# Optimization experiments

Measured on AMD Instinct MI355X. Metric: run time of the kernel, lower is better.

Reference implementation:

```python
import jax, jax.numpy as jnp
import numpy as np

N_NODES = 100000
N_EDGES = 1600000
F_IN = 32
HIDDEN = 32
N_CLASSES = 2


def setup_inputs() -> dict:
    key = jax.random.key(0)
    k0, k1, k2, k3 = jax.random.split(key, 4)
    x = jax.random.normal(k0, (N_NODES, F_IN), dtype=jnp.float32)
    edge_index = jax.random.randint(k1, (2, N_EDGES), 0, N_NODES, dtype=jnp.int64)
    W1 = jax.random.normal(k2, (F_IN, HIDDEN), dtype=jnp.float32) / np.sqrt(F_IN).astype(np.float32)
    b1 = jnp.zeros((HIDDEN,), dtype=jnp.float32)
    W2 = jax.random.normal(k3, (HIDDEN, N_CLASSES), dtype=jnp.float32) / np.sqrt(HIDDEN).astype(np.float32)
    b2 = jnp.zeros((N_CLASSES,), dtype=jnp.float32)
    return {"x": x, "edge_index": edge_index, "W1": W1, "b1": b1, "W2": W2, "b2": b2}


def _gcn_conv(x, W, b, src, dst, norm, n):
    # linear transform, gather from source nodes, scale by sym-norm, scatter-add to dst
    msg = (x @ W)[src] * norm[:, None]  # [E+N, out]
    return jax.ops.segment_sum(msg, dst, num_segments=n) + b


def reference(x, edge_index, W1, b1, W2, b2):
    n = x.shape[0]
    loops = jnp.arange(n, dtype=edge_index.dtype)
    src = jnp.concatenate([edge_index[0], loops])  # add self-loops (GCNConv default)
    dst = jnp.concatenate([edge_index[1], loops])
    deg = jax.ops.segment_sum(jnp.ones_like(dst, dtype=jnp.float32), dst, num_segments=n)
    dis = jax.lax.rsqrt(jnp.maximum(deg, 1.0))  # deg >= 1 because of self-loops
    norm = dis[src] * dis[dst]  # D^{-1/2} A_hat D^{-1/2} edge weights
    h = jax.nn.relu(_gcn_conv(x, W1, b1, src, dst, norm, n))
    # dropout is identity in eval mode (training=False)
    out = _gcn_conv(h, W2, b2, src, dst, norm, n)
    return jax.nn.log_softmax(out, axis=1)
```

## Files before the change

kernel.cpp:

```cpp
#include <hip/hip_runtime.h>
#include <hip/hip_fp16.h>
#include <math.h>

constexpr int N = 100000;
constexpr int E = 1600000;
constexpr int F = 32;
constexpr int C = 2;

constexpr int NBUCK = (N + 511) >> 9;
constexpr int CAPB  = 10240;
constexpr int CHUNK = 8192;
constexpr int NCHUNK = (E + CHUNK - 1) / CHUNK;

__global__ void k_detect(const int* __restrict__ ei, int* __restrict__ flag,
                         int* __restrict__ bcursor) {
    __shared__ int any;
    if (threadIdx.x == 0) any = 0;
    __syncthreads();
    int acc = 0;
    for (int i = threadIdx.x; i < 2048; i += blockDim.x)
        acc |= ei[2 * i + 1];
    if (acc) atomicOr(&any, 1);
    for (int i = threadIdx.x; i < NBUCK; i += blockDim.x) bcursor[i] = 0;
    __syncthreads();
    if (threadIdx.x == 0) flag[0] = any ? 0 : 1;
}

__device__ __forceinline__ int get_src(const int* ei, int e, int f64) {
    return f64 ? ei[2 * e] : ei[e];
}
__device__ __forceinline__ int get_dst(const int* ei, int e, int f64) {
    return f64 ? ei[2 * (E + e)] : ei[E + e];
}

__global__ void k_bucket(const int* __restrict__ ei, int* __restrict__ bcursor,
                         int* __restrict__ epk, const int* __restrict__ flag) {
    __shared__ int h[NBUCK];
    __shared__ int base[NBUCK];
    __shared__ int sS[CHUNK];
    __shared__ int sD[CHUNK];
    int tid = threadIdx.x;
    for (int i = tid; i < NBUCK; i += blockDim.x) h[i] = 0;
    __syncthreads();
    int f64 = flag[0];
    int e0 = blockIdx.x * CHUNK;
    int ne = min(E - e0, CHUNK);
    for (int i = tid; i < ne; i += blockDim.x) {
        int s = get_src(ei, e0 + i, f64);
        int d = get_dst(ei, e0 + i, f64);
        sS[i] = s;
        sD[i] = d;
        atomicAdd(&h[d >> 9], 1);
    }
    __syncthreads();
    for (int b = tid; b < NBUCK; b += blockDim.x) {
        if (h[b] > 0) base[b] = atomicAdd(&bcursor[b], h[b]);
        h[b] = 0;
    }
    __syncthreads();
    for (int i = tid; i < ne; i += blockDim.x) {
        int d = sD[i];
        int b = d >> 9;
        int r = atomicAdd(&h[b], 1);
        int pos = base[b] + r;
        if (pos < CAPB)
            epk[b * CAPB + pos] = ((d & 511) << 17) | sS[i];
    }
}

__global__ __launch_bounds__(512) void k_csr(
        const int* __restrict__ epk, const int* __restrict__ bcursor,
        int* __restrict__ rs, int* __restrict__ re,
        float* __restrict__ dis, int* __restrict__ colp) {
    __shared__ int hcnt[512];
    __shared__ int s[512];
    __shared__ int lcur[512];
    __shared__ int colseg[CAPB];
    int b = blockIdx.x;
    int tid = threadIdx.x;
    int n0 = b << 9;
    int nn = min(512, N - n0);
    int cbase = b * CAPB;
    int cnt = min(bcursor[b], CAPB);
    hcnt[tid] = 0;
    __syncthreads();
    for (int i = tid; i < cnt; i += 512)
        atomicAdd(&hcnt[epk[cbase + i] >> 17], 1);
    __syncthreads();
    s[tid] = hcnt[tid];
    __syncthreads();
    for (int off = 1; off < 512; off <<= 1) {
        int t = (tid >= off) ? s[tid - off] : 0;
        __syncthreads();
        s[tid] += t;
        __syncthreads();
    }
    int excl = s[tid] - hcnt[tid];
    lcur[tid] = excl;
    if (tid < nn) {
        rs[n0 + tid] = cbase + excl;
        re[n0 + tid] = cbase + excl + hcnt[tid];
        dis[n0 + tid] = rsqrtf((float)(hcnt[tid] + 1));
    }
    __syncthreads();
    for (int i = tid; i < cnt; i += 512) {
        int p = epk[cbase + i];
        int r = atomicAdd(&lcur[p >> 17], 1);
        colseg[r] = p & 0x1FFFF;
    }
    __syncthreads();
    for (int i = tid; i < cnt; i += 512) colp[cbase + i] = colseg[i];
}

__global__ void k_xw1(const float* __restrict__ x, const float* __restrict__ W1,
                      const float* __restrict__ dis, __half* __restrict__ t1h) {
    __shared__ float W1s[F * F];
    int tid = threadIdx.x;
    for (int i = tid; i < F * F; i += blockDim.x) W1s[i] = W1[i];
    __syncthreads();
    int lane = tid & 31;
    int node = (blockIdx.x * blockDim.x + tid) >> 5;
    if (node >= N) return;
    float xv = x[node * F + lane];
    float acc = 0.f;
#pragma unroll
    for (int k = 0; k < F; ++k) acc += __shfl(xv, k, 32) * W1s[k * F + lane];
    float v = acc * dis[node];
    float o = __shfl_xor(v, 1, 32);
    if (!(lane & 1))
        ((__half2*)t1h)[node * 16 + (lane >> 1)] = __floats2half2_rn(v, o);
}

__device__ __forceinline__ void acc8(float4& lo, float4& hi, const float4& r) {
    const __half2* hp = (const __half2*)&r;
    float2 f0 = __half22float2(hp[0]);
    float2 f1 = __half22float2(hp[1]);
    float2 f2 = __half22float2(hp[2]);
    float2 f3 = __half22float2(hp[3]);
    lo.x += f0.x; lo.y += f0.y; lo.z += f1.x; lo.w += f1.y;
    hi.x += f2.x; hi.y += f2.y; hi.z += f3.x; hi.w += f3.y;
}

__global__ void k_agg1(const int* __restrict__ rs, const int* __restrict__ re,
                       const int* __restrict__ colp, const __half* __restrict__ t1h,
                       const float* __restrict__ dis, const float* __restrict__ b1,
                       const float* __restrict__ W2, float* __restrict__ t2) {
    int tid = blockIdx.x * blockDim.x + threadIdx.x;
    int node = tid >> 2;
    if (node >= N) return;
    int lane = tid & 3;
    const float4* t1v = (const float4*)t1h;
    int start = rs[node], end = re[node];
    float4 lo0 = {0,0,0,0}, hi0 = {0,0,0,0};
    float4 lo1 = {0,0,0,0}, hi1 = {0,0,0,0};
    float4 lo2 = {0,0,0,0}, hi2 = {0,0,0,0};
    float4 lo3 = {0,0,0,0}, hi3 = {0,0,0,0};
    for (int base = start; base < end; base += 4) {
        int idx = base + lane;
        int sv = (idx < end) ? colp[idx] : 0;
        int cnt = end - base;
        if (cnt >= 4) {
            int i0 = __shfl(sv, 0, 4);
            int i1 = __shfl(sv, 1, 4);
            int i2 = __shfl(sv, 2, 4);
            int i3 = __shfl(sv, 3, 4);
            float4 r0 = t1v[i0 * 4 + lane];
            float4 r1 = t1v[i1 * 4 + lane];
            float4 r2 = t1v[i2 * 4 + lane];
            float4 r3 = t1v[i3 * 4 + lane];
            acc8(lo0, hi0, r0);
            acc8(lo1, hi1, r1);
            acc8(lo2, hi2, r2);
            acc8(lo3, hi3, r3);
        } else {
            for (int j = 0; j < cnt; ++j) {
                int ss = __shfl(sv, j, 4);
                float4 r = t1v[ss * 4 + lane];
                acc8(lo0, hi0, r);
            }
        }
    }
    float4 alo, ahi;
    alo.x = (lo0.x + lo1.x) + (lo2.x + lo3.x);
    alo.y = (lo0.y + lo1.y) + (lo2.y + lo3.y);
    alo.z = (lo0.z + lo1.z) + (lo2.z + lo3.z);
    alo.w = (lo0.w + lo1.w) + (lo2.w + lo3.w);
    ahi.x = (hi0.x + hi1.x) + (hi2.x + hi3.x);
    ahi.y = (hi0.y + hi1.y) + (hi2.y + hi3.y);
    ahi.z = (hi0.z + hi1.z) + (hi2.z + hi3.z);
    ahi.w = (hi0.w + hi1.w) + (hi2.w + hi3.w);
    float4 wself = t1v[node * 4 + lane];
    const __half2* sp = (const __half2*)&wself;
    float2 s0 = __half22float2(sp[0]);
    float2 s1 = __half22float2(sp[1]);
    float2 s2 = __half22float2(sp[2]);
    float2 s3 = __half22float2(sp[3]);
    float d = dis[node];
    int f0 = 8 * lane;
    float4 b1lo = *(const float4*)(b1 + f0);
    float4 b1hi = *(const float4*)(b1 + f0 + 4);
    float h0 = fmaxf(d * (alo.x + s0.x) + b1lo.x, 0.f);
    float h1 = fmaxf(d * (alo.y + s0.y) + b1lo.y, 0.f);
    float h2 = fmaxf(d * (alo.z + s1.x) + b1lo.z, 0.f);
    float h3 = fmaxf(d * (alo.w + s1.y) + b1lo.w, 0.f);
    float h4 = fmaxf(d * (ahi.x + s2.x) + b1hi.x, 0.f);
    float h5 = fmaxf(d * (ahi.y + s2.y) + b1hi.y, 0.f);
    float h6 = fmaxf(d * (ahi.z + s3.x) + b1hi.z, 0.f);
    float h7 = fmaxf(d * (ahi.w + s3.y) + b1hi.w, 0.f);
    const float4* w2v = (const float4*)W2;
    float4 q0 = w2v[4 * lane + 0];
    float4 q1 = w2v[4 * lane + 1];
    float4 q2 = w2v[4 * lane + 2];
    float4 q3 = w2v[4 * lane + 3];
    float p0 = h0 * q0.x + h1 * q0.z + h2 * q1.x + h3 * q1.z +
               h4 * q2.x + h5 * q2.z + h6 * q3.x + h7 * q3.z;
    float p1 = h0 * q0.y + h1 * q0.w + h2 * q1.y + h3 * q1.w +
               h4 * q2.y + h5 * q2.w + h6 * q3.y + h7 * q3.w;
    p0 += __shfl_xor(p0, 1, 4);
    p0 += __shfl_xor(p0, 2, 4);
    p1 += __shfl_xor(p1, 1, 4);
    p1 += __shfl_xor(p1, 2, 4);
    if (lane == 0) {
        float2 o;
        o.x = p0 * d;
        o.y = p1 * d;
        *(float2*)(t2 + node * C) = o;
    }
}

__global__ void k_agg2(const int* __restrict__ rs, const int* __restrict__ re,
                       const int* __restrict__ colp, const float* __restrict__ t2,
                       const float* __restrict__ dis, const float* __restrict__ b2,
                       float* __restrict__ out) {
    int tid = blockIdx.x * blockDim.x + threadIdx.x;
    int node = tid >> 4;
    if (node >= N) return;
    int lane = tid & 15;
    int start = rs[node], end = re[node];
    float a0 = 0.f, a1 = 0.f;
    for (int idx = start + lane; idx < end; idx += 16) {
        int s = colp[idx];
        float2 v = *(const float2*)(t2 + s * C);
        a0 += v.x;
        a1 += v.y;
    }
#pragma unroll
    for (int off = 8; off > 0; off >>= 1) {
        a0 += __shfl_xor(a0, off, 16);
        a1 += __shfl_xor(a1, off, 16);
    }
    if (lane == 0) {
        float d = dis[node];
        float2 self = *(const float2*)(t2 + node * C);
        float z0 = d * (a0 + self.x) + b2[0];
        float z1 = d * (a1 + self.y) + b2[1];
        float m = fmaxf(z0, z1);
        float l = m + logf(expf(z0 - m) + expf(z1 - m));
        float2 o;
        o.x = z0 - l;
        o.y = z1 - l;
        *(float2*)(out + node * C) = o;
    }
}

extern "C" void kernel_launch(void* const* d_in, const int* in_sizes, int n_in,
                              void* d_out, int out_size, void* d_ws, size_t ws_size,
                              hipStream_t stream) {
    const float* x  = (const float*)d_in[0];
    const int*   ei = (const int*)d_in[1];
    const float* W1 = (const float*)d_in[2];
    const float* b1 = (const float*)d_in[3];
    const float* W2 = (const float*)d_in[4];
    const float* b2 = (const float*)d_in[5];
    float* out = (float*)d_out;

    int* ws_i = (int*)d_ws;
    int*    epk     = ws_i;
    int*    colp    = epk + (size_t)NBUCK * CAPB;
    int*    rs      = colp + (size_t)NBUCK * CAPB;
    int*    re      = rs + N;
    float*  dis     = (float*)(re + N);
    float*  t2      = (float*)(dis + N);
    int*    bcursor = (int*)(t2 + (size_t)N * C);
    int*    flag    = bcursor + NBUCK;
    __half* t1h     = (__half*)epk;

    const int B = 256;
    k_detect<<<1, B, 0, stream>>>(ei, flag, bcursor);
    k_bucket<<<NCHUNK, B, 0, stream>>>(ei, bcursor, epk, flag);
    k_csr<<<NBUCK, 512, 0, stream>>>(epk, bcursor, rs, re, dis, colp);
    k_xw1<<<(N * 32 + B - 1) / B, B, 0, stream>>>(x, W1, dis, t1h);
    k_agg1<<<(N * 4 + B - 1) / B, B, 0, stream>>>(rs, re, colp, t1h, dis, b1, W2, t2);
    k_agg2<<<(N * 16 + B - 1) / B, B, 0, stream>>>(rs, re, colp, t2, dis, b2, out);
}
```

Measured before the change: 109.9 us.

## Fuse dtype detect into bucketing, accumulate agg1 in half2, shrink agg2 groups

Removes the separate detect kernel by having every bucket block check the edge-index dtype itself, and zeroes the bucket cursors with a memset instead. In agg1, neighbour features are summed in packed half2 accumulators and converted to float only at the end, cutting conversion ALU work at the risk of fp16 overflow or precision loss on high-degree nodes. agg2 now uses 8 lanes per node instead of 16. t1h gets its own workspace region rather than aliasing epk.

```diff
diff --git a/kernel.cpp b/kernel.cpp
--- a/kernel.cpp
+++ b/kernel.cpp
@@ -12,20 +12,6 @@
 constexpr int CHUNK = 8192;
 constexpr int NCHUNK = (E + CHUNK - 1) / CHUNK;
 
-__global__ void k_detect(const int* __restrict__ ei, int* __restrict__ flag,
-                         int* __restrict__ bcursor) {
-    __shared__ int any;
-    if (threadIdx.x == 0) any = 0;
-    __syncthreads();
-    int acc = 0;
-    for (int i = threadIdx.x; i < 2048; i += blockDim.x)
-        acc |= ei[2 * i + 1];
-    if (acc) atomicOr(&any, 1);
-    for (int i = threadIdx.x; i < NBUCK; i += blockDim.x) bcursor[i] = 0;
-    __syncthreads();
-    if (threadIdx.x == 0) flag[0] = any ? 0 : 1;
-}
-
 __device__ __forceinline__ int get_src(const int* ei, int e, int f64) {
     return f64 ? ei[2 * e] : ei[e];
 }
@@ -34,15 +20,21 @@
 }
 
 __global__ void k_bucket(const int* __restrict__ ei, int* __restrict__ bcursor,
-                         int* __restrict__ epk, const int* __restrict__ flag) {
+                         int* __restrict__ epk) {
     __shared__ int h[NBUCK];
     __shared__ int base[NBUCK];
     __shared__ int sS[CHUNK];
     __shared__ int sD[CHUNK];
+    __shared__ int sflag;
     int tid = threadIdx.x;
+    if (tid == 0) sflag = 0;
     for (int i = tid; i < NBUCK; i += blockDim.x) h[i] = 0;
     __syncthreads();
-    int f64 = flag[0];
+    int accf = 0;
+    for (int i = tid; i < 2048; i += blockDim.x) accf |= ei[2 * i + 1];
+    if (accf) atomicOr(&sflag, 1);
+    __syncthreads();
+    int f64 = sflag ? 0 : 1;
     int e0 = blockIdx.x * CHUNK;
     int ne = min(E - e0, CHUNK);
     for (int i = tid; i < ne; i += blockDim.x) {
@@ -131,14 +123,12 @@
         ((__half2*)t1h)[node * 16 + (lane >> 1)] = __floats2half2_rn(v, o);
 }
 
-__device__ __forceinline__ void acc8(float4& lo, float4& hi, const float4& r) {
+__device__ __forceinline__ void acch(__half2 (&a)[4], const float4& r) {
     const __half2* hp = (const __half2*)&r;
-    float2 f0 = __half22float2(hp[0]);
-    float2 f1 = __half22float2(hp[1]);
-    float2 f2 = __half22float2(hp[2]);
-    float2 f3 = __half22float2(hp[3]);
-    lo.x += f0.x; lo.y += f0.y; lo.z += f1.x; lo.w += f1.y;
-    hi.x += f2.x; hi.y += f2.y; hi.z += f3.x; hi.w += f3.y;
+    a[0] = __hadd2(a[0], hp[0]);
+    a[1] = __hadd2(a[1], hp[1]);
+    a[2] = __hadd2(a[2], hp[2]);
+    a[3] = __hadd2(a[3], hp[3]);
 }
 
 __global__ void k_agg1(const int* __restrict__ rs, const int* __restrict__ re,
@@ -151,10 +141,11 @@
     int lane = tid & 3;
     const float4* t1v = (const float4*)t1h;
     int start = rs[node], end = re[node];
-    float4 lo0 = {0,0,0,0}, hi0 = {0,0,0,0};
-    float4 lo1 = {0,0,0,0}, hi1 = {0,0,0,0};
-    float4 lo2 = {0,0,0,0}, hi2 = {0,0,0,0};
-    float4 lo3 = {0,0,0,0}, hi3 = {0,0,0,0};
+    __half2 z = __floats2half2_rn(0.f, 0.f);
+    __half2 a0[4] = {z, z, z, z};
+    __half2 a1[4] = {z, z, z, z};
+    __half2 a2[4] = {z, z, z, z};
+    __half2 a3[4] = {z, z, z, z};
     for (int base = start; base < end; base += 4) {
         int idx = base + lane;
         int sv = (idx < end) ? colp[idx] : 0;
@@ -168,27 +159,43 @@
             float4 r1 = t1v[i1 * 4 + lane];
             float4 r2 = t1v[i2 * 4 + lane];
             float4 r3 = t1v[i3 * 4 + lane];
-            acc8(lo0, hi0, r0);
-            acc8(lo1, hi1, r1);
-            acc8(lo2, hi2, r2);
-            acc8(lo3, hi3, r3);
+            acch(a0, r0);
+            acch(a1, r1);
+            acch(a2, r2);
+            acch(a3, r3);
         } else {
             for (int j = 0; j < cnt; ++j) {
                 int ss = __shfl(sv, j, 4);
                 float4 r = t1v[ss * 4 + lane];
-                acc8(lo0, hi0, r);
+                acch(a0, r);
             }
         }
     }
-    float4 alo, ahi;
-    alo.x = (lo0.x + lo1.x) + (lo2.x + lo3.x);
-    alo.y = (lo0.y + lo1.y) + (lo2.y + lo3.y);
-    alo.z = (lo0.z + lo1.z) + (lo2.z + lo3.z);
-    alo.w = (lo0.w + lo1.w) + (lo2.w + lo3.w);
-    ahi.x = (hi0.x + hi1.x) + (hi2.x + hi3.x);
-    ahi.y = (hi0.y + hi1.y) + (hi2.y + hi3.y);
-    ahi.z = (hi0.z + hi1.z) + (hi2.z + hi3.z);
-    ahi.w = (hi0.w + hi1.w) + (hi2.w + hi3.w);
+    float2 f0, f1, f2, f3;
+    {
+        float2 c0 = __half22float2(a0[0]), c1 = __half22float2(a1[0]);
+        float2 c2 = __half22float2(a2[0]), c3 = __half22float2(a3[0]);
+        f0.x = (c0.x + c1.x) + (c2.x + c3.x);
+        f0.y = (c0.y + c1.y) + (c2.y + c3.y);
+    }
+    {
+        float2 c0 = __half22float2(a0[1]), c1 = __half22float2(a1[1]);
+        float2 c2 = __half22float2(a2[1]), c3 = __half22float2(a3[1]);
+        f1.x = (c0.x + c1.x) + (c2.x + c3.x);
+        f1.y = (c0.y + c1.y) + (c2.y + c3.y);
+    }
+    {
+        float2 c0 = __half22float2(a0[2]), c1 = __half22float2(a1[2]);
+        float2 c2 = __half22float2(a2[2]), c3 = __half22float2(a3[2]);
+        f2.x = (c0.x + c1.x) + (c2.x + c3.x);
+        f2.y = (c0.y + c1.y) + (c2.y + c3.y);
+    }
+    {
+        float2 c0 = __half22float2(a0[3]), c1 = __half22float2(a1[3]);
+        float2 c2 = __half22float2(a2[3]), c3 = __half22float2(a3[3]);
+        f3.x = (c0.x + c1.x) + (c2.x + c3.x);
+        f3.y = (c0.y + c1.y) + (c2.y + c3.y);
+    }
     float4 wself = t1v[node * 4 + lane];
     const __half2* sp = (const __half2*)&wself;
     float2 s0 = __half22float2(sp[0]);
@@ -196,17 +203,17 @@
     float2 s2 = __half22float2(sp[2]);
     float2 s3 = __half22float2(sp[3]);
     float d = dis[node];
-    int f0 = 8 * lane;
-    float4 b1lo = *(const float4*)(b1 + f0);
-    float4 b1hi = *(const float4*)(b1 + f0 + 4);
-    float h0 = fmaxf(d * (alo.x + s0.x) + b1lo.x, 0.f);
-    float h1 = fmaxf(d * (alo.y + s0.y) + b1lo.y, 0.f);
-    float h2 = fmaxf(d * (alo.z + s1.x) + b1lo.z, 0.f);
-    float h3 = fmaxf(d * (alo.w + s1.y) + b1lo.w, 0.f);
-    float h4 = fmaxf(d * (ahi.x + s2.x) + b1hi.x, 0.f);
-    float h5 = fmaxf(d * (ahi.y + s2.y) + b1hi.y, 0.f);
-    float h6 = fmaxf(d * (ahi.z + s3.x) + b1hi.z, 0.f);
-    float h7 = fmaxf(d * (ahi.w + s3.y) + b1hi.w, 0.f);
+    int fb = 8 * lane;
+    float4 b1lo = *(const float4*)(b1 + fb);
+    float4 b1hi = *(const float4*)(b1 + fb + 4);
+    float h0 = fmaxf(d * (f0.x + s0.x) + b1lo.x, 0.f);
+    float h1 = fmaxf(d * (f0.y + s0.y) + b1lo.y, 0.f);
+    float h2 = fmaxf(d * (f1.x + s1.x) + b1lo.z, 0.f);
+    float h3 = fmaxf(d * (f1.y + s1.y) + b1lo.w, 0.f);
+    float h4 = fmaxf(d * (f2.x + s2.x) + b1hi.x, 0.f);
+    float h5 = fmaxf(d * (f2.y + s2.y) + b1hi.y, 0.f);
+    float h6 = fmaxf(d * (f3.x + s3.x) + b1hi.z, 0.f);
+    float h7 = fmaxf(d * (f3.y + s3.y) + b1hi.w, 0.f);
     const float4* w2v = (const float4*)W2;
     float4 q0 = w2v[4 * lane + 0];
     float4 q1 = w2v[4 * lane + 1];
@@ -233,21 +240,21 @@
                        const float* __restrict__ dis, const float* __restrict__ b2,
                        float* __restrict__ out) {
     int tid = blockIdx.x * blockDim.x + threadIdx.x;
-    int node = tid >> 4;
+    int node = tid >> 3;
     if (node >= N) return;
-    int lane = tid & 15;
+    int lane = tid & 7;
     int start = rs[node], end = re[node];
     float a0 = 0.f, a1 = 0.f;
-    for (int idx = start + lane; idx < end; idx += 16) {
+    for (int idx = start + lane; idx < end; idx += 8) {
         int s = colp[idx];
         float2 v = *(const float2*)(t2 + s * C);
         a0 += v.x;
         a1 += v.y;
     }
 #pragma unroll
-    for (int off = 8; off > 0; off >>= 1) {
-        a0 += __shfl_xor(a0, off, 16);
-        a1 += __shfl_xor(a1, off, 16);
+    for (int off = 4; off > 0; off >>= 1) {
+        a0 += __shfl_xor(a0, off, 8);
+        a1 += __shfl_xor(a1, off, 8);
     }
     if (lane == 0) {
         float d = dis[node];
@@ -280,16 +287,15 @@
     int*    rs      = colp + (size_t)NBUCK * CAPB;
     int*    re      = rs + N;
     float*  dis     = (float*)(re + N);
-    float*  t2      = (float*)(dis + N);
+    __half* t1h     = (__half*)(dis + N);
+    float*  t2      = (float*)(t1h + (size_t)N * F);
     int*    bcursor = (int*)(t2 + (size_t)N * C);
-    int*    flag    = bcursor + NBUCK;
-    __half* t1h     = (__half*)epk;
 
     const int B = 256;
-    k_detect<<<1, B, 0, stream>>>(ei, flag, bcursor);
-    k_bucket<<<NCHUNK, B, 0, stream>>>(ei, bcursor, epk, flag);
+    hipMemsetAsync(bcursor, 0, NBUCK * sizeof(int), stream);
+    k_bucket<<<NCHUNK, B, 0, stream>>>(ei, bcursor, epk);
     k_csr<<<NBUCK, 512, 0, stream>>>(epk, bcursor, rs, re, dis, colp);
     k_xw1<<<(N * 32 + B - 1) / B, B, 0, stream>>>(x, W1, dis, t1h);
     k_agg1<<<(N * 4 + B - 1) / B, B, 0, stream>>>(rs, re, colp, t1h, dis, b1, W2, t2);
-    k_agg2<<<(N * 16 + B - 1) / B, B, 0, stream>>>(rs, re, colp, t2, dis, b2, out);
-}
+    k_agg2<<<(N * 8 + B - 1) / B, B, 0, stream>>>(rs, re, colp, t2, dis, b2, out);
+}
```

Result: no change. 108.4 us (median of 2 runs) (-1.3%).
